# Optimization experiments

Hardware: AMD Instinct MI355X
Metric: run time of the kernel (lower is better)

The kernel has to match this reference:

```python
import jax, jax.numpy as jnp
import numpy as np

DIM = 96
HEADS = 4
WS = (2, 7, 7)      # window size (wd, wh, ww)
SS = (1, 3, 3)      # shift size
RES = (16, 56, 56)  # (D, H, W)
BATCH = 4
HIDDEN = 384        # mlp_ratio * dim
EPS = 1e-5


def _rel_pos_index(ws):
    wd, wh, ww = ws
    c = np.stack(np.meshgrid(np.arange(wd), np.arange(wh), np.arange(ww), indexing='ij')).reshape(3, -1)
    r = (c[:, :, None] - c[:, None, :]).transpose(1, 2, 0)  # (N, N, 3)
    r[..., 0] += wd - 1
    r[..., 1] += wh - 1
    r[..., 2] += ww - 1
    r[..., 0] *= (2 * wh - 1) * (2 * ww - 1)
    r[..., 1] *= (2 * ww - 1)
    return r.sum(-1)  # (N, N) int


def _attn_mask(res, ws, ss):
    D, H, W = res
    wd, wh, ww = ws
    sd, sh, sw = ss
    img = np.zeros((D, H, W), np.float32)
    cnt = 0
    for dsl in (slice(0, -wd), slice(-wd, -sd), slice(-sd, None)):
        for hsl in (slice(0, -wh), slice(-wh, -sh), slice(-sh, None)):
            for wsl in (slice(0, -ww), slice(-ww, -sw), slice(-sw, None)):
                img[dsl, hsl, wsl] = cnt
                cnt += 1
    N = wd * wh * ww
    m = img.reshape(D // wd, wd, H // wh, wh, W // ww, ww).transpose(0, 2, 4, 1, 3, 5).reshape(-1, N)
    am = m[:, None, :] - m[:, :, None]
    return np.where(am != 0, np.float32(-100.0), np.float32(0.0))  # (nW, N, N)


def setup_inputs() -> dict:
    key = jax.random.key(0)
    ks = jax.random.split(key, 8)
    s = 0.02
    return {
        'x': jax.random.normal(ks[0], (BATCH, DIM) + RES, jnp.float32),
        'gamma1': jnp.ones((DIM,), jnp.float32),
        'beta1': jnp.zeros((DIM,), jnp.float32),
        'gamma2': jnp.ones((DIM,), jnp.float32),
        'beta2': jnp.zeros((DIM,), jnp.float32),
        'qkv_w': jax.random.normal(ks[1], (DIM, 3 * DIM), jnp.float32) * s,
        'qkv_b': jnp.zeros((3 * DIM,), jnp.float32),
        'proj_w': jax.random.normal(ks[2], (DIM, DIM), jnp.float32) * s,
        'proj_b': jnp.zeros((DIM,), jnp.float32),
        'rpb_table': jax.random.normal(ks[3], ((2 * WS[0] - 1) * (2 * WS[1] - 1) * (2 * WS[2] - 1), HEADS), jnp.float32) * s,
        'fc1_w': jax.random.normal(ks[4], (DIM, HIDDEN), jnp.float32) * s,
        'fc1_b': jnp.zeros((HIDDEN,), jnp.float32),
        'fc2_w': jax.random.normal(ks[5], (HIDDEN, DIM), jnp.float32) * s,
        'fc2_b': jnp.zeros((DIM,), jnp.float32),
    }


def _layernorm(t, g, b):
    mu = t.mean(-1, keepdims=True)
    var = ((t - mu) ** 2).mean(-1, keepdims=True)
    return (t - mu) / jnp.sqrt(var + EPS) * g + b


def reference(x, gamma1, beta1, gamma2, beta2, qkv_w, qkv_b, proj_w, proj_b,
              rpb_table, fc1_w, fc1_b, fc2_w, fc2_b):
    B, C, D, H, W = x.shape
    wd, wh, ww = WS
    sd, sh, sw = SS
    N = wd * wh * ww
    nH = HEADS
    dh = C // nH

    rpi = jnp.asarray(_rel_pos_index(WS))          # (N, N) static
    mask = jnp.asarray(_attn_mask(RES, WS, SS))    # (nW, N, N) static
    nW = mask.shape[0]

    xl = jnp.transpose(x, (0, 2, 3, 4, 1))  # (B, D, H, W, C) channels-last

    # norm1 + cyclic shift
    h = _layernorm(xl, gamma1, beta1)
    h = jnp.roll(h, (-sd, -sh, -sw), axis=(1, 2, 3))

    # window partition -> (B*nW, N, C)
    win = h.reshape(B, D // wd, wd, H // wh, wh, W // ww, ww, C)
    win = win.transpose(0, 1, 3, 5, 2, 4, 6, 7).reshape(-1, N, C)

    # window attention
    qkv = (win @ qkv_w + qkv_b).reshape(-1, N, 3, nH, dh).transpose(2, 0, 3, 1, 4)
    q, k, v = qkv[0] * (dh ** -0.5), qkv[1], qkv[2]  # (B_, nH, N, dh)
    attn = jnp.einsum('bhnd,bhmd->bhnm', q, k)       # (B_, nH, N, N)
    rpb = rpb_table[rpi].transpose(2, 0, 1)          # (nH, N, N)
    attn = attn + rpb[None]
    attn = attn.reshape(B, nW, nH, N, N) + mask[None, :, None]
    attn = jax.nn.softmax(attn.reshape(-1, nH, N, N), axis=-1)
    out = jnp.einsum('bhnm,bhmd->bhnd', attn, v).transpose(0, 2, 1, 3).reshape(-1, N, C)
    out = out @ proj_w + proj_b

    # window reverse + reverse shift
    out = out.reshape(B, D // wd, H // wh, W // ww, wd, wh, ww, C)
    out = out.transpose(0, 1, 4, 2, 5, 3, 6, 7).reshape(B, D, H, W, C)
    out = jnp.roll(out, (sd, sh, sw), axis=(1, 2, 3))

    xl = xl + out  # residual 1

    # norm2 + 1x1-conv FFN (pointwise = matmul over channel)
    h2 = _layernorm(xl, gamma2, beta2)
    h2 = jax.nn.gelu(h2 @ fc1_w + fc1_b, approximate=False) @ fc2_w + fc2_b
    xl = xl + h2  # residual 2

    return jnp.transpose(xl, (0, 4, 1, 2, 3))  # back to (B, C, D, H, W)
```

## Files before the change

### kernel.cpp

```cpp
#include <hip/hip_runtime.h>
#include <hip/hip_bf16.h>
#include <cmath>

#define C_DIM 96
#define RES_D 16
#define RES_H 56
#define RES_W 56
#define BATCH 4
#define SPATIAL (RES_D*RES_H*RES_W)
#define NTOK (BATCH*SPATIAL)
#define NWIN_TOT 2048
#define EPS_LN 1e-5f
#define QSCALE 0.2041241452319315f

#define MPAD 112

#define OFF_P   0
#define OFF_Q   14336
#define OFF_K   28672
#define OFF_VT  43008
#define SM_TOT  59392

typedef float f32x4 __attribute__((ext_vector_type(4)));
typedef short s16x8 __attribute__((ext_vector_type(8)));
typedef unsigned u32x4 __attribute__((ext_vector_type(4)));
typedef unsigned u32x2 __attribute__((ext_vector_type(2)));
typedef unsigned short u16;

__device__ __forceinline__ u16 f2bf(float f) {
    unsigned u = __float_as_uint(f);
    u = (u + 0x7FFF + ((u >> 16) & 1)) >> 16;
    return (u16)u;
}
__device__ __forceinline__ int swzP(int r, int c) {
    return r * 128 + ((((c >> 3) ^ (r & 15)) << 3) | (c & 7));
}
__device__ __forceinline__ int swzQ(int r, int c) {
    return r * 32 + ((((c >> 3) ^ ((r >> 1) & 3)) << 3) | (c & 7));
}

__device__ __forceinline__ float wave_reduce_sum(float v) {
#pragma unroll
    for (int off = 32; off > 0; off >>= 1) v += __shfl_xor(v, off, 64);
    return v;
}

__global__ __launch_bounds__(256) void k_prep(
    const float* __restrict__ qkv_w, const float* __restrict__ proj_w,
    const float* __restrict__ fc1_w, const float* __restrict__ fc2_w,
    const float* __restrict__ rpb_table,
    u16* __restrict__ wq, u16* __restrict__ wp, u16* __restrict__ w1,
    u16* __restrict__ w2, float* __restrict__ rpbm) {
    int i = blockIdx.x * 256 + threadIdx.x;
    if (i < 27648) {
        int j = i / 96, c = i % 96;
        wq[i] = f2bf(qkv_w[c * 288 + j]);
    } else if (i < 36864) {
        int t = i - 27648; int j = t / 96, c = t % 96;
        wp[t] = f2bf(proj_w[c * 96 + j]);
    } else if (i < 73728) {
        int t = i - 36864; int j = t / 96, c = t % 96;
        w1[t] = f2bf(fc1_w[c * 384 + j]);
    } else if (i < 110592) {
        int t = i - 73728; int c = t / 384, j = t % 384;
        w2[t] = f2bf(fc2_w[j * 96 + c]);
    } else if (i < 176128) {
        int t = i - 110592;
        int h = t / 16384, r = t % 16384, n = r / 128, m = r % 128;
        float v;
        if (m >= 98) {
            v = -30000.0f;
        } else if (n >= 98) {
            v = 0.0f;
        } else {
            int dzn = n / 49, rn = n % 49, hyn = rn / 7, wxn = rn % 7;
            int dzm = m / 49, rm = m % 49, hym = rm / 7, wxm = rm % 7;
            int ridx = (dzn - dzm + 1) * 169 + (hyn - hym + 6) * 13 + (wxn - wxm + 6);
            v = rpb_table[ridx * 4 + h];
        }
        rpbm[t] = v;
    }
}

__global__ __launch_bounds__(256) void k_transpose_in(const float* __restrict__ x,
                                                      float* __restrict__ xl) {
    __shared__ float tile[32][33];
    const int b = blockIdx.z;
    const int s0 = blockIdx.x * 32;
    const int c0 = blockIdx.y * 32;
    const float* xb = x + (size_t)b * C_DIM * SPATIAL;
    float* xlb = xl + (size_t)b * SPATIAL * C_DIM;
    const int ts = threadIdx.x, tc = threadIdx.y;
#pragma unroll
    for (int i = 0; i < 32; i += 8)
        tile[tc + i][ts] = xb[(size_t)(c0 + tc + i) * SPATIAL + s0 + ts];
    __syncthreads();
#pragma unroll
    for (int i = 0; i < 32; i += 8)
        xlb[(size_t)(s0 + tc + i) * C_DIM + c0 + ts] = tile[ts][tc + i];
}

__global__ __launch_bounds__(448, 2) void k_win_attn(
    const float* __restrict__ xl, float* __restrict__ xl2,
    const float* __restrict__ g1, const float* __restrict__ b1,
    const u16* __restrict__ wqkv, const float* __restrict__ qkv_b,
    const u16* __restrict__ wproj, const float* __restrict__ proj_b,
    const float* __restrict__ rpbm) {
    __shared__ __align__(16) u16 sm[SM_TOT];
    __shared__ int s_gtok[MPAD];
    __shared__ int s_reg[MPAD];

    const int tid = threadIdx.x;
    const int lane = tid & 63;
    const int wv = tid >> 6;
    const int g4 = lane >> 4;
    const int c16 = lane & 15;
    const int mt = wv;

    const int wid = blockIdx.x;
    const int b = wid >> 9;
    const int rem = wid & 511;
    const int wdi = rem >> 6, whi = (rem >> 3) & 7, wwi = rem & 7;

    for (int i = tid; i < 7168; i += 448) {
        int c = 24 + (i & 7);
        int hb = (i >> 3) / 112;
        int r = (i >> 3) % 112;
        int base = (hb < 4) ? (OFF_Q + hb * 3584) : (OFF_K + (hb - 4) * 3584);
        sm[base + swzQ(r, c)] = 0;
    }
    for (int i = tid; i < 4096; i += 448) {
        int h = i >> 10, rr = 24 + ((i >> 7) & 7), c = i & 127;
        sm[OFF_VT + h * 4096 + swzP(rr, c)] = 0;
    }
    for (int i = tid; i < 1536; i += 448) {
        int h = i / 384, r = (i % 384) >> 4, c = 112 + (i & 15);
        sm[OFF_VT + h * 4096 + swzP(r, c)] = 0;
    }
    for (int i = tid; i < 1792; i += 448) {
        int r = i >> 4, c = 112 + (i & 15);
        sm[OFF_P + swzP(r, c)] = 0;
    }
    if (tid < MPAD) {
        if (tid < 98) {
            const int n = tid;
            const int dz = n / 49, r = n % 49, hy = r / 7, wx = r % 7;
            const int rd = wdi * 2 + dz, rh = whi * 7 + hy, rw = wwi * 7 + wx;
            int od = rd + 1; if (od >= RES_D) od -= RES_D;
            int oh = rh + 3; if (oh >= RES_H) oh -= RES_H;
            int ow = rw + 3; if (ow >= RES_W) ow -= RES_W;
            s_gtok[n] = ((b * RES_D + od) * RES_H + oh) * RES_W + ow;
            const int gd = (rd < 14) ? 0 : (rd < 15 ? 1 : 2);
            const int gh = (rh < 49) ? 0 : (rh < 53 ? 1 : 2);
            const int gw = (rw < 49) ? 0 : (rw < 53 ? 1 : 2);
            s_reg[n] = gd * 9 + gh * 3 + gw;
        } else { s_gtok[tid] = 0; s_reg[tid] = -1; }
    }
    __syncthreads();

    const int myrow = mt * 16 + c16;
    const float live = (myrow < 98) ? 1.0f : 0.0f;
    u32x4 xa[3];
    {
        const float* src = xl + (size_t)s_gtok[myrow] * C_DIM;
        f32x4 xv0 = *(const f32x4*)(src + 0 * 32 + g4 * 8);
        f32x4 xv1 = *(const f32x4*)(src + 0 * 32 + g4 * 8 + 4);
        f32x4 xv2 = *(const f32x4*)(src + 1 * 32 + g4 * 8);
        f32x4 xv3 = *(const f32x4*)(src + 1 * 32 + g4 * 8 + 4);
        f32x4 xv4 = *(const f32x4*)(src + 2 * 32 + g4 * 8);
        f32x4 xv5 = *(const f32x4*)(src + 2 * 32 + g4 * 8 + 4);
        float lsum = (xv0[0]+xv0[1]+xv0[2]+xv0[3]) + (xv1[0]+xv1[1]+xv1[2]+xv1[3])
                   + (xv2[0]+xv2[1]+xv2[2]+xv2[3]) + (xv3[0]+xv3[1]+xv3[2]+xv3[3])
                   + (xv4[0]+xv4[1]+xv4[2]+xv4[3]) + (xv5[0]+xv5[1]+xv5[2]+xv5[3]);
        lsum += __shfl_xor(lsum, 16, 64);
        lsum += __shfl_xor(lsum, 32, 64);
        const float mu = lsum * (1.0f / 96.0f);
        f32x4 d0 = xv0 - mu, d1 = xv1 - mu, d2 = xv2 - mu,
              d3 = xv3 - mu, d4 = xv4 - mu, d5 = xv5 - mu;
        float lvv = (d0[0]*d0[0]+d0[1]*d0[1]+d0[2]*d0[2]+d0[3]*d0[3])
                  + (d1[0]*d1[0]+d1[1]*d1[1]+d1[2]*d1[2]+d1[3]*d1[3])
                  + (d2[0]*d2[0]+d2[1]*d2[1]+d2[2]*d2[2]+d2[3]*d2[3])
                  + (d3[0]*d3[0]+d3[1]*d3[1]+d3[2]*d3[2]+d3[3]*d3[3])
                  + (d4[0]*d4[0]+d4[1]*d4[1]+d4[2]*d4[2]+d4[3]*d4[3])
                  + (d5[0]*d5[0]+d5[1]*d5[1]+d5[2]*d5[2]+d5[3]*d5[3]);
        lvv += __shfl_xor(lvv, 16, 64);
        lvv += __shfl_xor(lvv, 32, 64);
        const float rstd = rsqrtf(lvv * (1.0f / 96.0f) + EPS_LN) * live;
#pragma unroll
        for (int ks = 0; ks < 3; ++ks) {
            const f32x4 ea = (ks == 0) ? d0 : (ks == 1) ? d2 : d4;
            const f32x4 eb = (ks == 0) ? d1 : (ks == 1) ? d3 : d5;
            f32x4 ga = *(const f32x4*)(g1 + ks * 32 + g4 * 8);
            f32x4 gb = *(const f32x4*)(g1 + ks * 32 + g4 * 8 + 4);
            f32x4 ba = *(const f32x4*)(b1 + ks * 32 + g4 * 8);
            f32x4 bb = *(const f32x4*)(b1 + ks * 32 + g4 * 8 + 4);
            f32x4 y0 = ea * rstd * ga + ba * live;
            f32x4 y1 = eb * rstd * gb + bb * live;
            xa[ks][0] = (unsigned)f2bf(y0[0]) | ((unsigned)f2bf(y0[1]) << 16);
            xa[ks][1] = (unsigned)f2bf(y0[2]) | ((unsigned)f2bf(y0[3]) << 16);
            xa[ks][2] = (unsigned)f2bf(y1[0]) | ((unsigned)f2bf(y1[1]) << 16);
            xa[ks][3] = (unsigned)f2bf(y1[2]) | ((unsigned)f2bf(y1[3]) << 16);
        }
    }

#pragma unroll
    for (int sel = 0; sel < 3; ++sel) {
#pragma unroll
        for (int t = 0; t < 6; ++t) {
            const int nt = sel * 6 + t;
            f32x4 acc = {0.f, 0.f, 0.f, 0.f};
#pragma unroll
            for (int ks = 0; ks < 3; ++ks) {
                s16x8 a = __builtin_bit_cast(s16x8, xa[ks]);
                s16x8 bw = *(const s16x8*)(wqkv + (size_t)(nt * 16 + c16) * 96 + ks * 32 + g4 * 8);
                acc = __builtin_amdgcn_mfma_f32_16x16x32_bf16(a, bw, acc, 0, 0, 0);
            }
            const float bias = qkv_b[nt * 16 + c16];
            float v0 = acc[0] + bias, v1 = acc[1] + bias, v2 = acc[2] + bias, v3 = acc[3] + bias;
            if (sel == 0) { v0 *= QSCALE; v1 *= QSCALE; v2 *= QSCALE; v3 *= QSCALE; }
            const int j96 = t * 16 + c16;
            const int h = j96 / 24, d = j96 - h * 24;
            const int row0 = mt * 16 + g4 * 4;
            if (sel == 0) {
                sm[OFF_Q + h * 3584 + swzQ(row0 + 0, d)] = f2bf(v0);
                sm[OFF_Q + h * 3584 + swzQ(row0 + 1, d)] = f2bf(v1);
                sm[OFF_Q + h * 3584 + swzQ(row0 + 2, d)] = f2bf(v2);
                sm[OFF_Q + h * 3584 + swzQ(row0 + 3, d)] = f2bf(v3);
            } else if (sel == 1) {
                sm[OFF_K + h * 3584 + swzQ(row0 + 0, d)] = f2bf(v0);
                sm[OFF_K + h * 3584 + swzQ(row0 + 1, d)] = f2bf(v1);
                sm[OFF_K + h * 3584 + swzQ(row0 + 2, d)] = f2bf(v2);
                sm[OFF_K + h * 3584 + swzQ(row0 + 3, d)] = f2bf(v3);
            } else {
                sm[OFF_VT + h * 4096 + swzP(d, row0 + 0)] = f2bf(v0);
                sm[OFF_VT + h * 4096 + swzP(d, row0 + 1)] = f2bf(v1);
                sm[OFF_VT + h * 4096 + swzP(d, row0 + 2)] = f2bf(v2);
                sm[OFF_VT + h * 4096 + swzP(d, row0 + 3)] = f2bf(v3);
            }
        }
    }
    __syncthreads();

    unsigned ogp[4][2][2];
    const int rbase = mt * 16 + g4 * 4;
    int rgs[4];
#pragma unroll
    for (int r = 0; r < 4; ++r) rgs[r] = s_reg[rbase + r];
#pragma unroll
    for (int h = 0; h < 4; ++h) {
        const s16x8 aq = *(const s16x8*)&sm[OFF_Q + h * 3584 + swzQ(mt * 16 + c16, g4 * 8)];
        const float* rh = rpbm + h * 16384;
        float smr[4] = {0.f, 0.f, 0.f, 0.f};
#pragma unroll
        for (int nt = 0; nt < 7; ++nt) {
            s16x8 bk = *(const s16x8*)&sm[OFF_K + h * 3584 + swzQ(nt * 16 + c16, g4 * 8)];
            f32x4 z = {0.f, 0.f, 0.f, 0.f};
            f32x4 sc = __builtin_amdgcn_mfma_f32_16x16x32_bf16(aq, bk, z, 0, 0, 0);
            const int col = nt * 16 + c16;
            const int creg = s_reg[col];
#pragma unroll
            for (int r = 0; r < 4; ++r) {
                float s = sc[r] + rh[(rbase + r) * 128 + col];
                if (rgs[r] != creg) s -= 100.0f;
                const float e = __expf(s);
                sc[r] = e;
                smr[r] += e;
            }
            sm[OFF_P + swzP(rbase + 0, col)] = f2bf(sc[0]);
            sm[OFF_P + swzP(rbase + 1, col)] = f2bf(sc[1]);
            sm[OFF_P + swzP(rbase + 2, col)] = f2bf(sc[2]);
            sm[OFF_P + swzP(rbase + 3, col)] = f2bf(sc[3]);
        }
#pragma unroll
        for (int r = 0; r < 4; ++r) {
#pragma unroll
            for (int m = 1; m <= 8; m <<= 1) smr[r] += __shfl_xor(smr[r], m, 64);
            smr[r] = 1.0f / fmaxf(smr[r], 1e-30f);
        }
#pragma unroll
        for (int dt = 0; dt < 2; ++dt) {
            f32x4 acc = {0.f, 0.f, 0.f, 0.f};
#pragma unroll
            for (int ks = 0; ks < 4; ++ks) {
                s16x8 ap = *(const s16x8*)&sm[OFF_P + swzP(mt * 16 + c16, ks * 32 + g4 * 8)];
                s16x8 bv = *(const s16x8*)&sm[OFF_VT + h * 4096 + swzP(dt * 16 + c16, ks * 32 + g4 * 8)];
                acc = __builtin_amdgcn_mfma_f32_16x16x32_bf16(ap, bv, acc, 0, 0, 0);
            }
            ogp[h][dt][0] = (unsigned)f2bf(acc[0] * smr[0]) | ((unsigned)f2bf(acc[1] * smr[1]) << 16);
            ogp[h][dt][1] = (unsigned)f2bf(acc[2] * smr[2]) | ((unsigned)f2bf(acc[3] * smr[3]) << 16);
        }
    }

#pragma unroll
    for (int h = 0; h < 4; ++h) {
#pragma unroll
        for (int dt = 0; dt < 2; ++dt) {
            const int d = dt * 16 + c16;
            if (d < 24) {
                const int col = h * 24 + d;
#pragma unroll
                for (int rp = 0; rp < 2; ++rp) {
                    const unsigned u = ogp[h][dt][rp];
                    const int row0 = mt * 16 + g4 * 4 + rp * 2;
                    sm[OFF_P + swzP(row0, col)] = (u16)u;
                    sm[OFF_P + swzP(row0 + 1, col)] = (u16)(u >> 16);
                }
            }
        }
    }

#pragma unroll
    for (int nt = 0; nt < 6; ++nt) {
        f32x4 acc = {0.f, 0.f, 0.f, 0.f};
#pragma unroll
        for (int ks = 0; ks < 3; ++ks) {
            s16x8 a = *(const s16x8*)&sm[OFF_P + swzP(mt * 16 + c16, ks * 32 + g4 * 8)];
            s16x8 bw = *(const s16x8*)(wproj + (size_t)(nt * 16 + c16) * 96 + ks * 32 + g4 * 8);
            acc = __builtin_amdgcn_mfma_f32_16x16x32_bf16(a, bw, acc, 0, 0, 0);
        }
        const int col = nt * 16 + c16;
        const float pb = proj_b[col];
#pragma unroll
        for (int r = 0; r < 4; ++r) {
            const int row = mt * 16 + g4 * 4 + r;
            if (row < 98) {
                const size_t base = (size_t)s_gtok[row] * C_DIM + col;
                xl2[base] = xl[base] + acc[r] + pb;
            }
        }
    }
}

__global__ __launch_bounds__(256, 3) void k_ffn(
    const float* __restrict__ xl2, float* __restrict__ out,
    const float* __restrict__ g2, const float* __restrict__ b2,
    const u16* __restrict__ w1, const float* __restrict__ fc1_b,
    const u16* __restrict__ w2, const float* __restrict__ fc2_b) {
    __shared__ __align__(16) u16 sg[64 * 384];
    float* s_res = (float*)sg;

    const int tid = threadIdx.x;
    const int lane = tid & 63;
    const int wave = tid >> 6;
    const int g4 = lane >> 4, c16 = lane & 15;
    const int mg = wave & 1;
    const int nh = wave >> 1;
    const int t0 = blockIdx.x * 64;

    u32x4 xa[2][3];
#pragma unroll
    for (int g = 0; g < 2; ++g) {
        const int tok = mg * 32 + g * 16 + c16;
        const float* src = xl2 + (size_t)(t0 + tok) * C_DIM;
        f32x4 xv0 = *(const f32x4*)(src + 0 * 32 + g4 * 8);
        f32x4 xv1 = *(const f32x4*)(src + 0 * 32 + g4 * 8 + 4);
        f32x4 xv2 = *(const f32x4*)(src + 1 * 32 + g4 * 8);
        f32x4 xv3 = *(const f32x4*)(src + 1 * 32 + g4 * 8 + 4);
        f32x4 xv4 = *(const f32x4*)(src + 2 * 32 + g4 * 8);
        f32x4 xv5 = *(const f32x4*)(src + 2 * 32 + g4 * 8 + 4);
        float lsum = (xv0[0]+xv0[1]+xv0[2]+xv0[3]) + (xv1[0]+xv1[1]+xv1[2]+xv1[3])
                   + (xv2[0]+xv2[1]+xv2[2]+xv2[3]) + (xv3[0]+xv3[1]+xv3[2]+xv3[3])
                   + (xv4[0]+xv4[1]+xv4[2]+xv4[3]) + (xv5[0]+xv5[1]+xv5[2]+xv5[3]);
        lsum += __shfl_xor(lsum, 16, 64);
        lsum += __shfl_xor(lsum, 32, 64);
        const float mu = lsum * (1.0f / 96.0f);
        f32x4 d0 = xv0 - mu, d1 = xv1 - mu, d2 = xv2 - mu,
              d3 = xv3 - mu, d4 = xv4 - mu, d5 = xv5 - mu;
        float lvv = (d0[0]*d0[0]+d0[1]*d0[1]+d0[2]*d0[2]+d0[3]*d0[3])
                  + (d1[0]*d1[0]+d1[1]*d1[1]+d1[2]*d1[2]+d1[3]*d1[3])
                  + (d2[0]*d2[0]+d2[1]*d2[1]+d2[2]*d2[2]+d2[3]*d2[3])
                  + (d3[0]*d3[0]+d3[1]*d3[1]+d3[2]*d3[2]+d3[3]*d3[3])
                  + (d4[0]*d4[0]+d4[1]*d4[1]+d4[2]*d4[2]+d4[3]*d4[3])
                  + (d5[0]*d5[0]+d5[1]*d5[1]+d5[2]*d5[2]+d5[3]*d5[3]);
        lvv += __shfl_xor(lvv, 16, 64);
        lvv += __shfl_xor(lvv, 32, 64);
        const float rstd = rsqrtf(lvv * (1.0f / 96.0f) + EPS_LN);
#pragma unroll
        for (int ks = 0; ks < 3; ++ks) {
            const f32x4 ea = (ks == 0) ? d0 : (ks == 1) ? d2 : d4;
            const f32x4 eb = (ks == 0) ? d1 : (ks == 1) ? d3 : d5;
            f32x4 ga = *(const f32x4*)(g2 + ks * 32 + g4 * 8);
            f32x4 gb = *(const f32x4*)(g2 + ks * 32 + g4 * 8 + 4);
            f32x4 ba = *(const f32x4*)(b2 + ks * 32 + g4 * 8);
            f32x4 bb = *(const f32x4*)(b2 + ks * 32 + g4 * 8 + 4);
            f32x4 y0 = ea * rstd * ga + ba;
            f32x4 y1 = eb * rstd * gb + bb;
            xa[g][ks][0] = (unsigned)f2bf(y0[0]) | ((unsigned)f2bf(y0[1]) << 16);
            xa[g][ks][1] = (unsigned)f2bf(y0[2]) | ((unsigned)f2bf(y0[3]) << 16);
            xa[g][ks][2] = (unsigned)f2bf(y1[0]) | ((unsigned)f2bf(y1[1]) << 16);
            xa[g][ks][3] = (unsigned)f2bf(y1[2]) | ((unsigned)f2bf(y1[3]) << 16);
        }
    }

#pragma unroll 1
    for (int i = 0; i < 12; ++i) {
        const int nt = nh * 12 + i;
        f32x4 acc0 = {0.f, 0.f, 0.f, 0.f};
        f32x4 acc1 = {0.f, 0.f, 0.f, 0.f};
#pragma unroll
        for (int ks = 0; ks < 3; ++ks) {
            s16x8 aw = *(const s16x8*)(w1 + (size_t)(nt * 16 + c16) * 96 + ks * 32 + g4 * 8);
            acc0 = __builtin_amdgcn_mfma_f32_16x16x32_bf16(aw, __builtin_bit_cast(s16x8, xa[0][ks]), acc0, 0, 0, 0);
            acc1 = __builtin_amdgcn_mfma_f32_16x16x32_bf16(aw, __builtin_bit_cast(s16x8, xa[1][ks]), acc1, 0, 0, 0);
        }
        const f32x4 bias = *(const f32x4*)(fc1_b + nt * 16 + g4 * 4);
#pragma unroll
        for (int g = 0; g < 2; ++g) {
            const f32x4 acc = (g == 0) ? acc0 : acc1;
            const int tok = mg * 32 + g * 16 + c16;
            float gv[4];
#pragma unroll
            for (int r = 0; r < 4; ++r) {
                const float v = acc[r] + bias[r];
                gv[r] = 0.5f * v * (1.0f + erff(v * 0.70710678118654752f));
            }
            const unsigned lo = (unsigned)f2bf(gv[0]) | ((unsigned)f2bf(gv[1]) << 16);
            const unsigned hi = (unsigned)f2bf(gv[2]) | ((unsigned)f2bf(gv[3]) << 16);
            const int chunk = (2 * nt + (g4 >> 1)) ^ (tok & 15);
            u32x2 pk = {lo, hi};
            *(u32x2*)&sg[tok * 384 + chunk * 8 + (g4 & 1) * 4] = pk;
        }
    }
    __syncthreads();

    f32x4 facc[3][2];
    const int tokA = mg * 32 + c16;
    const int tokB = tokA + 16;
#pragma unroll 1
    for (int i = 0; i < 3; ++i) {
        const int nt = nh * 3 + i;
        f32x4 a0 = {0.f, 0.f, 0.f, 0.f};
        f32x4 a1 = {0.f, 0.f, 0.f, 0.f};
#pragma unroll
        for (int ks = 0; ks < 12; ++ks) {
            s16x8 aw = *(const s16x8*)(w2 + (size_t)(nt * 16 + c16) * 384 + ks * 32 + g4 * 8);
            s16x8 bg0 = *(const s16x8*)&sg[tokA * 384 + (((ks * 4 + g4) ^ (tokA & 15)) << 3)];
            s16x8 bg1 = *(const s16x8*)&sg[tokB * 384 + (((ks * 4 + g4) ^ (tokB & 15)) << 3)];
            a0 = __builtin_amdgcn_mfma_f32_16x16x32_bf16(aw, bg0, a0, 0, 0, 0);
            a1 = __builtin_amdgcn_mfma_f32_16x16x32_bf16(aw, bg1, a1, 0, 0, 0);
        }
        const f32x4 bias = *(const f32x4*)(fc2_b + nt * 16 + g4 * 4);
        const f32x4 resA = *(const f32x4*)(xl2 + (size_t)(t0 + tokA) * C_DIM + nt * 16 + g4 * 4);
        const f32x4 resB = *(const f32x4*)(xl2 + (size_t)(t0 + tokB) * C_DIM + nt * 16 + g4 * 4);
        facc[i][0] = a0 + bias + resA;
        facc[i][1] = a1 + bias + resB;
    }
    __syncthreads();

#pragma unroll
    for (int i = 0; i < 3; ++i) {
        const int nt = nh * 3 + i;
#pragma unroll
        for (int g = 0; g < 2; ++g) {
            const int tok = mg * 32 + g * 16 + c16;
#pragma unroll
            for (int r = 0; r < 4; ++r)
                s_res[tok * 97 + nt * 16 + g4 * 4 + r] = facc[i][g][r];
        }
    }
    __syncthreads();

    const int bb = t0 / SPATIAL;
    const int sbase = t0 % SPATIAL;
    for (int e = tid; e < 1536; e += 256) {
        const int c = e >> 4, tq = e & 15;
        f32x4 v;
        v[0] = s_res[(tq * 4 + 0) * 97 + c];
        v[1] = s_res[(tq * 4 + 1) * 97 + c];
        v[2] = s_res[(tq * 4 + 2) * 97 + c];
        v[3] = s_res[(tq * 4 + 3) * 97 + c];
        *(f32x4*)&out[((size_t)bb * C_DIM + c) * SPATIAL + sbase + tq * 4] = v;
    }
}

extern "C" void kernel_launch(void* const* d_in, const int* in_sizes, int n_in,
                              void* d_out, int out_size, void* d_ws, size_t ws_size,
                              hipStream_t stream) {
    const float* x      = (const float*)d_in[0];
    const float* g1     = (const float*)d_in[1];
    const float* be1    = (const float*)d_in[2];
    const float* g2     = (const float*)d_in[3];
    const float* be2    = (const float*)d_in[4];
    const float* qkv_w  = (const float*)d_in[5];
    const float* qkv_b  = (const float*)d_in[6];
    const float* proj_w = (const float*)d_in[7];
    const float* proj_b = (const float*)d_in[8];
    const float* rpb    = (const float*)d_in[9];
    const float* fc1_w  = (const float*)d_in[10];
    const float* fc1_b  = (const float*)d_in[11];
    const float* fc2_w  = (const float*)d_in[12];
    const float* fc2_b  = (const float*)d_in[13];
    float* out = (float*)d_out;

    float* xl  = (float*)d_ws;
    float* xl2 = xl + (size_t)NTOK * C_DIM;
    u16* wq = (u16*)(xl2 + (size_t)NTOK * C_DIM);
    u16* wp = wq + 27648;
    u16* w1 = wp + 9216;
    u16* w2 = w1 + 36864;
    float* rpbm = (float*)(w2 + 36864);

    k_prep<<<688, 256, 0, stream>>>(qkv_w, proj_w, fc1_w, fc2_w, rpb, wq, wp, w1, w2, rpbm);
    k_transpose_in<<<dim3(SPATIAL / 32, C_DIM / 32, BATCH), dim3(32, 8), 0, stream>>>(x, xl);
    k_win_attn<<<NWIN_TOT, 448, 0, stream>>>(xl, xl2, g1, be1, wq, qkv_b, wp, proj_b, rpbm);
    k_ffn<<<NTOK / 64, 256, 0, stream>>>(xl2, out, g2, be2, w1, fc1_b, w2, fc2_b);
}
```

Measured before the change: 378.0 us.

## Swap MFMA operand order in window attention for vectorized LDS and global stores

In the window-attention kernel, several MFMAs now take their operands in swapped order (weights or K as A, activations as B), so each lane holds four consecutive columns of a single token. That lets Q/K, P, the attention output and the projection result go out as packed 8-byte LDS stores and 16-byte global loads and stores, replacing scattered 2-byte and 4-byte ones. The shift mask is precomputed once per lane as a bitmask, replacing per-element compares in the softmax loop. The row-sum reduction simplifies to two shuffles. Correctness depends on the new swizzled index mapping staying consistent between writers and readers.

```diff
diff --git a/kernel.cpp b/kernel.cpp
--- a/kernel.cpp
+++ b/kernel.cpp
@@ -31,6 +31,9 @@
     unsigned u = __float_as_uint(f);
     u = (u + 0x7FFF + ((u >> 16) & 1)) >> 16;
     return (u16)u;
+}
+__device__ __forceinline__ unsigned pk2(float lo, float hi) {
+    return (unsigned)f2bf(lo) | ((unsigned)f2bf(hi) << 16);
 }
 __device__ __forceinline__ int swzP(int r, int c) {
     return r * 128 + ((((c >> 3) ^ (r & 15)) << 3) | (c & 7));
@@ -107,8 +110,8 @@
     const u16* __restrict__ wproj, const float* __restrict__ proj_b,
     const float* __restrict__ rpbm) {
     __shared__ __align__(16) u16 sm[SM_TOT];
-    __shared__ int s_gtok[MPAD];
-    __shared__ int s_reg[MPAD];
+    __shared__ __align__(16) int s_gtok[MPAD];
+    __shared__ __align__(16) int s_reg[MPAD];
 
     const int tid = threadIdx.x;
     const int lane = tid & 63;
@@ -158,11 +161,12 @@
     }
     __syncthreads();
 
-    const int myrow = mt * 16 + c16;
-    const float live = (myrow < 98) ? 1.0f : 0.0f;
+    const int mytok = mt * 16 + c16;
+    const float live = (mytok < 98) ? 1.0f : 0.0f;
+
     u32x4 xa[3];
     {
-        const float* src = xl + (size_t)s_gtok[myrow] * C_DIM;
+        const float* src = xl + (size_t)s_gtok[mytok] * C_DIM;
         f32x4 xv0 = *(const f32x4*)(src + 0 * 32 + g4 * 8);
         f32x4 xv1 = *(const f32x4*)(src + 0 * 32 + g4 * 8 + 4);
         f32x4 xv2 = *(const f32x4*)(src + 1 * 32 + g4 * 8);
@@ -196,10 +200,10 @@
             f32x4 bb = *(const f32x4*)(b1 + ks * 32 + g4 * 8 + 4);
             f32x4 y0 = ea * rstd * ga + ba * live;
             f32x4 y1 = eb * rstd * gb + bb * live;
-            xa[ks][0] = (unsigned)f2bf(y0[0]) | ((unsigned)f2bf(y0[1]) << 16);
-            xa[ks][1] = (unsigned)f2bf(y0[2]) | ((unsigned)f2bf(y0[3]) << 16);
-            xa[ks][2] = (unsigned)f2bf(y1[0]) | ((unsigned)f2bf(y1[1]) << 16);
-            xa[ks][3] = (unsigned)f2bf(y1[2]) | ((unsigned)f2bf(y1[3]) << 16);
+            xa[ks][0] = pk2(y0[0], y0[1]);
+            xa[ks][1] = pk2(y0[2], y0[3]);
+            xa[ks][2] = pk2(y1[0], y1[1]);
+            xa[ks][3] = pk2(y1[2], y1[3]);
         }
     }
 
@@ -209,85 +213,84 @@
         for (int t = 0; t < 6; ++t) {
             const int nt = sel * 6 + t;
             f32x4 acc = {0.f, 0.f, 0.f, 0.f};
-#pragma unroll
-            for (int ks = 0; ks < 3; ++ks) {
-                s16x8 a = __builtin_bit_cast(s16x8, xa[ks]);
-                s16x8 bw = *(const s16x8*)(wqkv + (size_t)(nt * 16 + c16) * 96 + ks * 32 + g4 * 8);
-                acc = __builtin_amdgcn_mfma_f32_16x16x32_bf16(a, bw, acc, 0, 0, 0);
+            if (sel < 2) {
+#pragma unroll
+                for (int ks = 0; ks < 3; ++ks) {
+                    s16x8 bw = *(const s16x8*)(wqkv + (size_t)(nt * 16 + c16) * 96 + ks * 32 + g4 * 8);
+                    acc = __builtin_amdgcn_mfma_f32_16x16x32_bf16(bw, __builtin_bit_cast(s16x8, xa[ks]), acc, 0, 0, 0);
+                }
+                const int jb = t * 16 + g4 * 4;
+                const f32x4 b4 = *(const f32x4*)(qkv_b + sel * 96 + jb);
+                f32x4 v = acc + b4;
+                if (sel == 0) { v[0] *= QSCALE; v[1] *= QSCALE; v[2] *= QSCALE; v[3] *= QSCALE; }
+                const int h = jb / 24, db = jb - h * 24;
+                u32x2 pkv = { pk2(v[0], v[1]), pk2(v[2], v[3]) };
+                const int base = (sel == 0 ? OFF_Q : OFF_K) + h * 3584;
+                *(u32x2*)&sm[base + swzQ(mytok, db)] = pkv;
+            } else {
+#pragma unroll
+                for (int ks = 0; ks < 3; ++ks) {
+                    s16x8 bw = *(const s16x8*)(wqkv + (size_t)(nt * 16 + c16) * 96 + ks * 32 + g4 * 8);
+                    acc = __builtin_amdgcn_mfma_f32_16x16x32_bf16(__builtin_bit_cast(s16x8, xa[ks]), bw, acc, 0, 0, 0);
+                }
+                const int j96 = t * 16 + c16;
+                const float bias = qkv_b[192 + j96];
+                const int h = j96 / 24, d = j96 - h * 24;
+                const int row0 = mt * 16 + g4 * 4;
+                f32x4 v = acc + bias;
+                u32x2 pkv = { pk2(v[0], v[1]), pk2(v[2], v[3]) };
+                *(u32x2*)&sm[OFF_VT + h * 4096 + swzP(d, row0)] = pkv;
             }
-            const float bias = qkv_b[nt * 16 + c16];
-            float v0 = acc[0] + bias, v1 = acc[1] + bias, v2 = acc[2] + bias, v3 = acc[3] + bias;
-            if (sel == 0) { v0 *= QSCALE; v1 *= QSCALE; v2 *= QSCALE; v3 *= QSCALE; }
-            const int j96 = t * 16 + c16;
-            const int h = j96 / 24, d = j96 - h * 24;
-            const int row0 = mt * 16 + g4 * 4;
-            if (sel == 0) {
-                sm[OFF_Q + h * 3584 + swzQ(row0 + 0, d)] = f2bf(v0);
-                sm[OFF_Q + h * 3584 + swzQ(row0 + 1, d)] = f2bf(v1);
-                sm[OFF_Q + h * 3584 + swzQ(row0 + 2, d)] = f2bf(v2);
-                sm[OFF_Q + h * 3584 + swzQ(row0 + 3, d)] = f2bf(v3);
-            } else if (sel == 1) {
-                sm[OFF_K + h * 3584 + swzQ(row0 + 0, d)] = f2bf(v0);
-                sm[OFF_K + h * 3584 + swzQ(row0 + 1, d)] = f2bf(v1);
-                sm[OFF_K + h * 3584 + swzQ(row0 + 2, d)] = f2bf(v2);
-                sm[OFF_K + h * 3584 + swzQ(row0 + 3, d)] = f2bf(v3);
-            } else {
-                sm[OFF_VT + h * 4096 + swzP(d, row0 + 0)] = f2bf(v0);
-                sm[OFF_VT + h * 4096 + swzP(d, row0 + 1)] = f2bf(v1);
-                sm[OFF_VT + h * 4096 + swzP(d, row0 + 2)] = f2bf(v2);
-                sm[OFF_VT + h * 4096 + swzP(d, row0 + 3)] = f2bf(v3);
-            }
-        }
-    }
-    __syncthreads();
+        }
+    }
+    __syncthreads();
+
+    const int rgq = s_reg[mytok];
+    unsigned mbits = 0;
+#pragma unroll
+    for (int nt = 0; nt < 7; ++nt) {
+        const int4 cr = *(const int4*)&s_reg[nt * 16 + g4 * 4];
+        mbits |= (unsigned)(cr.x != rgq) << (nt * 4 + 0);
+        mbits |= (unsigned)(cr.y != rgq) << (nt * 4 + 1);
+        mbits |= (unsigned)(cr.z != rgq) << (nt * 4 + 2);
+        mbits |= (unsigned)(cr.w != rgq) << (nt * 4 + 3);
+    }
 
     unsigned ogp[4][2][2];
-    const int rbase = mt * 16 + g4 * 4;
-    int rgs[4];
-#pragma unroll
-    for (int r = 0; r < 4; ++r) rgs[r] = s_reg[rbase + r];
 #pragma unroll
     for (int h = 0; h < 4; ++h) {
-        const s16x8 aq = *(const s16x8*)&sm[OFF_Q + h * 3584 + swzQ(mt * 16 + c16, g4 * 8)];
-        const float* rh = rpbm + h * 16384;
-        float smr[4] = {0.f, 0.f, 0.f, 0.f};
+        const s16x8 aq = *(const s16x8*)&sm[OFF_Q + h * 3584 + swzQ(mytok, g4 * 8)];
+        const float* rq = rpbm + h * 16384 + mytok * 128;
+        float smr = 0.f;
 #pragma unroll
         for (int nt = 0; nt < 7; ++nt) {
-            s16x8 bk = *(const s16x8*)&sm[OFF_K + h * 3584 + swzQ(nt * 16 + c16, g4 * 8)];
+            s16x8 ak = *(const s16x8*)&sm[OFF_K + h * 3584 + swzQ(nt * 16 + c16, g4 * 8)];
             f32x4 z = {0.f, 0.f, 0.f, 0.f};
-            f32x4 sc = __builtin_amdgcn_mfma_f32_16x16x32_bf16(aq, bk, z, 0, 0, 0);
-            const int col = nt * 16 + c16;
-            const int creg = s_reg[col];
-#pragma unroll
-            for (int r = 0; r < 4; ++r) {
-                float s = sc[r] + rh[(rbase + r) * 128 + col];
-                if (rgs[r] != creg) s -= 100.0f;
-                const float e = __expf(s);
-                sc[r] = e;
-                smr[r] += e;
-            }
-            sm[OFF_P + swzP(rbase + 0, col)] = f2bf(sc[0]);
-            sm[OFF_P + swzP(rbase + 1, col)] = f2bf(sc[1]);
-            sm[OFF_P + swzP(rbase + 2, col)] = f2bf(sc[2]);
-            sm[OFF_P + swzP(rbase + 3, col)] = f2bf(sc[3]);
-        }
-#pragma unroll
-        for (int r = 0; r < 4; ++r) {
-#pragma unroll
-            for (int m = 1; m <= 8; m <<= 1) smr[r] += __shfl_xor(smr[r], m, 64);
-            smr[r] = 1.0f / fmaxf(smr[r], 1e-30f);
-        }
+            f32x4 sc = __builtin_amdgcn_mfma_f32_16x16x32_bf16(ak, aq, z, 0, 0, 0);
+            const f32x4 rv = *(const f32x4*)&rq[nt * 16 + g4 * 4];
+            float s0 = sc[0] + rv[0] - 100.0f * (float)((mbits >> (nt * 4 + 0)) & 1u);
+            float s1 = sc[1] + rv[1] - 100.0f * (float)((mbits >> (nt * 4 + 1)) & 1u);
+            float s2 = sc[2] + rv[2] - 100.0f * (float)((mbits >> (nt * 4 + 2)) & 1u);
+            float s3 = sc[3] + rv[3] - 100.0f * (float)((mbits >> (nt * 4 + 3)) & 1u);
+            const float e0 = __expf(s0), e1 = __expf(s1), e2 = __expf(s2), e3 = __expf(s3);
+            smr += (e0 + e1) + (e2 + e3);
+            u32x2 pkv = { pk2(e0, e1), pk2(e2, e3) };
+            *(u32x2*)&sm[OFF_P + swzP(mytok, nt * 16 + g4 * 4)] = pkv;
+        }
+        smr += __shfl_xor(smr, 16, 64);
+        smr += __shfl_xor(smr, 32, 64);
+        const float iq = 1.0f / fmaxf(smr, 1e-30f);
 #pragma unroll
         for (int dt = 0; dt < 2; ++dt) {
             f32x4 acc = {0.f, 0.f, 0.f, 0.f};
 #pragma unroll
             for (int ks = 0; ks < 4; ++ks) {
-                s16x8 ap = *(const s16x8*)&sm[OFF_P + swzP(mt * 16 + c16, ks * 32 + g4 * 8)];
-                s16x8 bv = *(const s16x8*)&sm[OFF_VT + h * 4096 + swzP(dt * 16 + c16, ks * 32 + g4 * 8)];
-                acc = __builtin_amdgcn_mfma_f32_16x16x32_bf16(ap, bv, acc, 0, 0, 0);
+                s16x8 av = *(const s16x8*)&sm[OFF_VT + h * 4096 + swzP(dt * 16 + c16, ks * 32 + g4 * 8)];
+                s16x8 bp = *(const s16x8*)&sm[OFF_P + swzP(mt * 16 + c16, ks * 32 + g4 * 8)];
+                acc = __builtin_amdgcn_mfma_f32_16x16x32_bf16(av, bp, acc, 0, 0, 0);
             }
-            ogp[h][dt][0] = (unsigned)f2bf(acc[0] * smr[0]) | ((unsigned)f2bf(acc[1] * smr[1]) << 16);
-            ogp[h][dt][1] = (unsigned)f2bf(acc[2] * smr[2]) | ((unsigned)f2bf(acc[3] * smr[3]) << 16);
+            ogp[h][dt][0] = pk2(acc[0] * iq, acc[1] * iq);
+            ogp[h][dt][1] = pk2(acc[2] * iq, acc[3] * iq);
         }
     }
 
@@ -295,38 +298,29 @@
     for (int h = 0; h < 4; ++h) {
 #pragma unroll
         for (int dt = 0; dt < 2; ++dt) {
-            const int d = dt * 16 + c16;
-            if (d < 24) {
-                const int col = h * 24 + d;
-#pragma unroll
-                for (int rp = 0; rp < 2; ++rp) {
-                    const unsigned u = ogp[h][dt][rp];
-                    const int row0 = mt * 16 + g4 * 4 + rp * 2;
-                    sm[OFF_P + swzP(row0, col)] = (u16)u;
-                    sm[OFF_P + swzP(row0 + 1, col)] = (u16)(u >> 16);
-                }
+            const int db = dt * 16 + g4 * 4;
+            if (db < 24) {
+                u32x2 v = { ogp[h][dt][0], ogp[h][dt][1] };
+                *(u32x2*)&sm[OFF_P + swzP(mytok, h * 24 + db)] = v;
             }
         }
     }
 
+    const int gq = s_gtok[mytok];
 #pragma unroll
     for (int nt = 0; nt < 6; ++nt) {
         f32x4 acc = {0.f, 0.f, 0.f, 0.f};
 #pragma unroll
         for (int ks = 0; ks < 3; ++ks) {
-            s16x8 a = *(const s16x8*)&sm[OFF_P + swzP(mt * 16 + c16, ks * 32 + g4 * 8)];
-            s16x8 bw = *(const s16x8*)(wproj + (size_t)(nt * 16 + c16) * 96 + ks * 32 + g4 * 8);
-            acc = __builtin_amdgcn_mfma_f32_16x16x32_bf16(a, bw, acc, 0, 0, 0);
-        }
-        const int col = nt * 16 + c16;
-        const float pb = proj_b[col];
-#pragma unroll
-        for (int r = 0; r < 4; ++r) {
-            const int row = mt * 16 + g4 * 4 + r;
-            if (row < 98) {
-                const size_t base = (size_t)s_gtok[row] * C_DIM + col;
-                xl2[base] = xl[base] + acc[r] + pb;
-            }
+            s16x8 aw = *(const s16x8*)(wproj + (size_t)(nt * 16 + c16) * 96 + ks * 32 + g4 * 8);
+            s16x8 bo = *(const s16x8*)&sm[OFF_P + swzP(mt * 16 + c16, ks * 32 + g4 * 8)];
+            acc = __builtin_amdgcn_mfma_f32_16x16x32_bf16(aw, bo, acc, 0, 0, 0);
+        }
+        if (mytok < 98) {
+            const int cb = nt * 16 + g4 * 4;
+            const f32x4 pb4 = *(const f32x4*)(proj_b + cb);
+            const f32x4 res = *(const f32x4*)(xl + (size_t)gq * C_DIM + cb);
+            *(f32x4*)(xl2 + (size_t)gq * C_DIM + cb) = acc + pb4 + res;
         }
     }
 }
@@ -385,10 +379,10 @@
             f32x4 bb = *(const f32x4*)(b2 + ks * 32 + g4 * 8 + 4);
             f32x4 y0 = ea * rstd * ga + ba;
             f32x4 y1 = eb * rstd * gb + bb;
-            xa[g][ks][0] = (unsigned)f2bf(y0[0]) | ((unsigned)f2bf(y0[1]) << 16);
-            xa[g][ks][1] = (unsigned)f2bf(y0[2]) | ((unsigned)f2bf(y0[3]) << 16);
-            xa[g][ks][2] = (unsigned)f2bf(y1[0]) | ((unsigned)f2bf(y1[1]) << 16);
-            xa[g][ks][3] = (unsigned)f2bf(y1[2]) | ((unsigned)f2bf(y1[3]) << 16);
+            xa[g][ks][0] = pk2(y0[0], y0[1]);
+            xa[g][ks][1] = pk2(y0[2], y0[3]);
+            xa[g][ks][2] = pk2(y1[0], y1[1]);
+            xa[g][ks][3] = pk2(y1[2], y1[3]);
         }
     }
 
@@ -414,10 +408,8 @@
                 const float v = acc[r] + bias[r];
                 gv[r] = 0.5f * v * (1.0f + erff(v * 0.70710678118654752f));
             }
-            const unsigned lo = (unsigned)f2bf(gv[0]) | ((unsigned)f2bf(gv[1]) << 16);
-            const unsigned hi = (unsigned)f2bf(gv[2]) | ((unsigned)f2bf(gv[3]) << 16);
             const int chunk = (2 * nt + (g4 >> 1)) ^ (tok & 15);
-            u32x2 pk = {lo, hi};
+            u32x2 pk = { pk2(gv[0], gv[1]), pk2(gv[2], gv[3]) };
             *(u32x2*)&sg[tok * 384 + chunk * 8 + (g4 & 1) * 4] = pk;
         }
     }
```

Result: faster. 354.4 us, median of 2 (-6.2%).
